# Optimization experiments

Measured on AMD Instinct MI355X. Metric: run time of the kernel, lower is better.

## Reference

```python
import jax, jax.numpy as jnp
import numpy as np

TEMP = 0.5
EPS = 1e-12  # matches torch F.normalize default eps


def _l2_normalize(x):
    n = jnp.sqrt(jnp.sum(x * x, axis=1, keepdims=True))
    return x / jnp.maximum(n, EPS)


def setup_inputs() -> dict:
    key = jax.random.key(0)
    k1, k2 = jax.random.split(key)
    B, D = 4096, 256
    return {
        "x_i": jax.random.normal(k1, (B, D), dtype=jnp.float32),
        "x_j": jax.random.normal(k2, (B, D), dtype=jnp.float32),
    }


def reference(x_i, x_j):
    B = x_i.shape[0]
    z = jnp.concatenate([_l2_normalize(x_i), _l2_normalize(x_j)], axis=0)  # [2B, D]
    # cosine similarity of normalized vectors == plain matmul
    sim = z @ z.T  # [2B, 2B]
    pos = jnp.concatenate([jnp.diagonal(sim, B), jnp.diagonal(sim, -B)], axis=0)  # [2B]
    neg_mask = 1.0 - jnp.eye(2 * B, dtype=sim.dtype)
    denom = jnp.sum(neg_mask * jnp.exp(sim / TEMP), axis=1)  # [2B]
    # -log(exp(pos/T) / denom) = -pos/T + log(denom)
    loss = jnp.sum(-(pos / TEMP) + jnp.log(denom)) / (2 * B)
    return loss
```

## Files before the change

### kernel.cpp

```cpp
#include <hip/hip_runtime.h>
#include <hip/hip_bf16.h>

#define B_ROWS 4096
#define NROWS  8192
#define D      256
#define NSEG   32
#define NBLK2  1024
#define TPP    130

typedef __attribute__((ext_vector_type(4))) float floatx4;

__global__ __launch_bounds__(256) void norm_pos_kernel(
    const float* __restrict__ xi, const float* __restrict__ xj,
    unsigned char* __restrict__ z, float* __restrict__ pos,
    float* __restrict__ rowsum, float* __restrict__ out,
    unsigned int* __restrict__ counter) {
    int gt = blockIdx.x * 256 + threadIdx.x;
    if (gt < NROWS) rowsum[gt] = 0.f;
    if (gt == 0) { out[0] = 0.f; counter[0] = 0u; }

    int p    = blockIdx.x * 4 + (threadIdx.x >> 6);
    int lane = threadIdx.x & 63;
    float4 v1 = ((const float4*)(xi + (size_t)p * D))[lane];
    float4 v2 = ((const float4*)(xj + (size_t)p * D))[lane];
    float ss1 = v1.x * v1.x + v1.y * v1.y + v1.z * v1.z + v1.w * v1.w;
    float ss2 = v2.x * v2.x + v2.y * v2.y + v2.z * v2.z + v2.w * v2.w;
#pragma unroll
    for (int off = 32; off > 0; off >>= 1) {
        ss1 += __shfl_xor(ss1, off);
        ss2 += __shfl_xor(ss2, off);
    }
    float sc1 = 1.0f / fmaxf(sqrtf(ss1), 1e-12f);
    float sc2 = 1.0f / fmaxf(sqrtf(ss2), 1e-12f);

    float n1x = v1.x * sc1, n1y = v1.y * sc1, n1z = v1.z * sc1, n1w = v1.w * sc1;
    float n2x = v2.x * sc2, n2y = v2.y * sc2, n2z = v2.z * sc2, n2w = v2.w * sc2;

    float dp = n1x * n2x + n1y * n2y + n1z * n2z + n1w * n2w;
#pragma unroll
    for (int off = 32; off > 0; off >>= 1) dp += __shfl_xor(dp, off);
    if (lane == 0) { pos[p] = dp; pos[p + B_ROWS] = dp; }

    int q1 = __builtin_amdgcn_cvt_pk_fp8_f32(n1x, n1y, 0, false);
    q1     = __builtin_amdgcn_cvt_pk_fp8_f32(n1z, n1w, q1, true);
    int q2 = __builtin_amdgcn_cvt_pk_fp8_f32(n2x, n2y, 0, false);
    q2     = __builtin_amdgcn_cvt_pk_fp8_f32(n2z, n2w, q2, true);
    ((int*)(z + (size_t)p * D))[lane]            = q1;
    ((int*)(z + (size_t)(p + B_ROWS) * D))[lane] = q2;
}

__global__ __launch_bounds__(256, 4) void sim_rowsum_kernel(
    const unsigned char* __restrict__ z, float* __restrict__ rowsum,
    const float* __restrict__ pos, unsigned int* __restrict__ counter,
    float* __restrict__ out) {
    __shared__ __align__(16) int4 Bbuf[2][1024];
    __shared__ unsigned int done_s;
    __shared__ float sdata[4];

    const int tid  = threadIdx.x;
    const int lane = tid & 63;
    const int w    = tid >> 6;
    const int lm   = lane & 15;
    const int lg   = lane >> 4;

    const int s  = blockIdx.x >> 5;
    const int q  = blockIdx.x & 31;
    const int L0 = 128 - 2 * s;
    const int cb = (q * TPP) >> 5;
    const int ce = ((q + 1) * TPP) >> 5;

    const int scol  = tid >> 2;
    const int spart = tid & 3;

    long long a[8][2];
    floatx4 acc[2][4];
    float rsacc[2][4];
    int4 pf[4];

#pragma unroll
    for (int mi = 0; mi < 2; mi++)
#pragma unroll
        for (int r = 0; r < 4; r++) rsacc[mi][r] = 0.f;

    auto decode = [&](int c, int& strip, int& colbase, int& cloc) {
        if (c < L0) { strip = s;      cloc = c; }
        else        { strip = 63 - s; cloc = c - L0; }
        colbase = strip * 128 + cloc * 64;
    };

    auto loadA = [&](int strip) {
#pragma unroll
        for (int kk = 0; kk < 8; kk++)
#pragma unroll
            for (int mi = 0; mi < 2; mi++)
                a[kk][mi] = *(const long long*)(
                    z + (size_t)(strip * 128 + w * 32 + mi * 16 + lm) * D +
                    kk * 32 + lg * 8);
    };

    auto flushRs = [&](int strip) {
#pragma unroll
        for (int mi = 0; mi < 2; mi++)
#pragma unroll
            for (int r = 0; r < 4; r++) {
                float v = rsacc[mi][r];
                v += __shfl_xor(v, 1); v += __shfl_xor(v, 2);
                v += __shfl_xor(v, 4); v += __shfl_xor(v, 8);
                if (lm == 0)
                    atomicAdd(&rowsum[strip * 128 + w * 32 + mi * 16 + lg * 4 + r], v);
                rsacc[mi][r] = 0.f;
            }
    };

    auto fetch = [&](int colbase) {
        const unsigned char* p = z + (size_t)(colbase + scol) * D + spart * 16;
#pragma unroll
        for (int j = 0; j < 4; j++) pf[j] = *(const int4*)(p + j * 64);
    };
    auto writeB = [&](int buf) {
#pragma unroll
        for (int j = 0; j < 4; j++)
            Bbuf[buf][(spart + 4 * j) * 64 + scol] = pf[j];
    };

    int strip, colbase, cloc;
    decode(cb, strip, colbase, cloc);
    int curstrip = strip;
    fetch(colbase);
    writeB(0);
    loadA(strip);
    __syncthreads();

    for (int c = cb; c < ce; c++) {
        const int buf = (c - cb) & 1;
        decode(c, strip, colbase, cloc);

        const bool hn = (c + 1 < ce);
        if (hn) {
            int ns, ncb, ncl;
            decode(c + 1, ns, ncb, ncl);
            fetch(ncb);
        }
        if (strip != curstrip) {
            flushRs(curstrip);
            loadA(strip);
            curstrip = strip;
        }

#pragma unroll
        for (int mi = 0; mi < 2; mi++)
#pragma unroll
            for (int ni = 0; ni < 4; ni++)
                acc[mi][ni] = (floatx4){0.f, 0.f, 0.f, 0.f};

        const char* bbase = (const char*)Bbuf[buf];
#pragma unroll
        for (int kk = 0; kk < 8; kk++) {
            long long b[4];
#pragma unroll
            for (int ni = 0; ni < 4; ni++)
                b[ni] = *(const long long*)(
                    bbase + (((kk * 2 + (lg >> 1)) * 64 + ni * 16 + lm) * 16) +
                    (lg & 1) * 8);
#pragma unroll
            for (int mi = 0; mi < 2; mi++)
#pragma unroll
                for (int ni = 0; ni < 4; ni++)
                    acc[mi][ni] = __builtin_amdgcn_mfma_f32_16x16x32_fp8_fp8(
                        a[kk][mi], b[ni], acc[mi][ni], 0, 0, 0);
        }

        const bool diagreg = (cloc < 2);
        float cs[4] = {0.f, 0.f, 0.f, 0.f};
        if (diagreg) {
            const int rowb = strip * 128 + w * 32 + lg * 4;
#pragma unroll
            for (int mi = 0; mi < 2; mi++)
#pragma unroll
                for (int ni = 0; ni < 4; ni++) {
                    const int gcol = colbase + ni * 16 + lm;
#pragma unroll
                    for (int r = 0; r < 4; r++) {
                        int grow = rowb + mi * 16 + r;
                        float e = (grow == gcol) ? 0.f
                                                 : __expf(2.0f * acc[mi][ni][r]);
                        rsacc[mi][r] += e;
                    }
                }
        } else {
#pragma unroll
            for (int mi = 0; mi < 2; mi++)
#pragma unroll
                for (int ni = 0; ni < 4; ni++)
#pragma unroll
                    for (int r = 0; r < 4; r++) {
                        float e = __expf(2.0f * acc[mi][ni][r]);
                        rsacc[mi][r] += e;
                        cs[ni]      += e;
                    }
#pragma unroll
            for (int ni = 0; ni < 4; ni++) {
                float v = cs[ni];
                v += __shfl_xor(v, 16); v += __shfl_xor(v, 32);
                if (lane < 16)
                    atomicAdd(&rowsum[colbase + ni * 16 + lane], v);
            }
        }

        if (hn) {
            writeB(buf ^ 1);
            __syncthreads();
        }
    }
    flushRs(curstrip);

    __syncthreads();
    if (tid == 0) {
        __threadfence();
        done_s = atomicAdd(counter, 1u);
    }
    __syncthreads();
    if (done_s == (unsigned int)(NBLK2 - 1)) {
        __threadfence();
        float acc_l = 0.f;
#pragma unroll 4
        for (int r = tid; r < NROWS; r += 256) {
            float rsv = __hip_atomic_load(&rowsum[r], __ATOMIC_RELAXED,
                                          __HIP_MEMORY_SCOPE_AGENT);
            acc_l += -2.0f * pos[r] + logf(rsv);
        }
#pragma unroll
        for (int off = 32; off > 0; off >>= 1) acc_l += __shfl_xor(acc_l, off);
        if (lane == 0) sdata[w] = acc_l;
        __syncthreads();
        if (tid == 0)
            out[0] = (sdata[0] + sdata[1] + sdata[2] + sdata[3]) / (float)NROWS;
    }
}

extern "C" void kernel_launch(void* const* d_in, const int* in_sizes, int n_in,
                              void* d_out, int out_size, void* d_ws, size_t ws_size,
                              hipStream_t stream) {
    const float* xi = (const float*)d_in[0];
    const float* xj = (const float*)d_in[1];
    float* out      = (float*)d_out;

    char* ws        = (char*)d_ws;
    unsigned char* z = (unsigned char*)ws;
    float* rowsum   = (float*)(ws + (size_t)NROWS * D);
    float* pos      = rowsum + NROWS;
    unsigned int* counter = (unsigned int*)(pos + NROWS);

    norm_pos_kernel<<<B_ROWS / 4, 256, 0, stream>>>(xi, xj, z, pos,
                                                    rowsum, out, counter);
    sim_rowsum_kernel<<<NBLK2, 256, 0, stream>>>(z, rowsum, pos, counter, out);
}
```

Baseline: 123.1 us.

## Restructure sim kernel to one 128x128 upper-triangle tile per block with swizzled LDS

```diff
diff --git a/kernel.cpp b/kernel.cpp
--- a/kernel.cpp
+++ b/kernel.cpp
@@ -4,9 +4,8 @@
 #define B_ROWS 4096
 #define NROWS  8192
 #define D      256
-#define NSEG   32
-#define NBLK2  1024
-#define TPP    130
+#define TILES  64
+#define NPAIRS 2080
 
 typedef __attribute__((ext_vector_type(4))) float floatx4;
 
@@ -49,11 +48,12 @@
     ((int*)(z + (size_t)(p + B_ROWS) * D))[lane] = q2;
 }
 
-__global__ __launch_bounds__(256, 4) void sim_rowsum_kernel(
+__global__ __launch_bounds__(256, 2) void sim_rowsum_kernel(
     const unsigned char* __restrict__ z, float* __restrict__ rowsum,
     const float* __restrict__ pos, unsigned int* __restrict__ counter,
     float* __restrict__ out) {
-    __shared__ __align__(16) int4 Bbuf[2][1024];
+    __shared__ __align__(16) char Ab[32768];
+    __shared__ __align__(16) char Bb[32768];
     __shared__ unsigned int done_s;
     __shared__ float sdata[4];
 
@@ -63,156 +63,132 @@
     const int lm   = lane & 15;
     const int lg   = lane >> 4;
 
-    const int s  = blockIdx.x >> 5;
-    const int q  = blockIdx.x & 31;
-    const int L0 = 128 - 2 * s;
-    const int cb = (q * TPP) >> 5;
-    const int ce = ((q + 1) * TPP) >> 5;
-
-    const int scol  = tid >> 2;
-    const int spart = tid & 3;
-
-    long long a[8][2];
-    floatx4 acc[2][4];
-    float rsacc[2][4];
-    int4 pf[4];
-
-#pragma unroll
-    for (int mi = 0; mi < 2; mi++)
-#pragma unroll
-        for (int r = 0; r < 4; r++) rsacc[mi][r] = 0.f;
-
-    auto decode = [&](int c, int& strip, int& colbase, int& cloc) {
-        if (c < L0) { strip = s;      cloc = c; }
-        else        { strip = 63 - s; cloc = c - L0; }
-        colbase = strip * 128 + cloc * 64;
-    };
-
-    auto loadA = [&](int strip) {
-#pragma unroll
-        for (int kk = 0; kk < 8; kk++)
-#pragma unroll
-            for (int mi = 0; mi < 2; mi++)
-                a[kk][mi] = *(const long long*)(
-                    z + (size_t)(strip * 128 + w * 32 + mi * 16 + lm) * D +
-                    kk * 32 + lg * 8);
-    };
-
-    auto flushRs = [&](int strip) {
-#pragma unroll
-        for (int mi = 0; mi < 2; mi++)
-#pragma unroll
-            for (int r = 0; r < 4; r++) {
-                float v = rsacc[mi][r];
-                v += __shfl_xor(v, 1); v += __shfl_xor(v, 2);
-                v += __shfl_xor(v, 4); v += __shfl_xor(v, 8);
-                if (lm == 0)
-                    atomicAdd(&rowsum[strip * 128 + w * 32 + mi * 16 + lg * 4 + r], v);
-                rsacc[mi][r] = 0.f;
+    int bid = blockIdx.x;
+    int ti  = (int)((129.0 - sqrt(16641.0 - 8.0 * (double)bid)) * 0.5);
+    while (ti > 0 && ti * TILES - ti * (ti - 1) / 2 > bid) ti--;
+    while ((ti + 1) * TILES - (ti + 1) * ti / 2 <= bid) ti++;
+    int tj = ti + (bid - (ti * TILES - ti * (ti - 1) / 2));
+    const int m0 = ti * 128, n0 = tj * 128;
+    const bool diag = (ti == tj);
+
+    const int wr = (w & 1) * 64;
+    const int wc = (w >> 1) * 64;
+
+    {
+        const int rb    = tid >> 2;
+        const int spart = tid & 3;
+        int4 pa[2][4], pb[2][4];
+#pragma unroll
+        for (int p = 0; p < 2; p++) {
+            const int row = rb + p * 64;
+            const unsigned char* pza = z + (size_t)(m0 + row) * D;
+            const unsigned char* pzb = z + (size_t)(n0 + row) * D;
+#pragma unroll
+            for (int j = 0; j < 4; j++) {
+                pa[p][j] = *(const int4*)(pza + spart * 16 + j * 64);
+                pb[p][j] = *(const int4*)(pzb + spart * 16 + j * 64);
             }
-    };
-
-    auto fetch = [&](int colbase) {
-        const unsigned char* p = z + (size_t)(colbase + scol) * D + spart * 16;
-#pragma unroll
-        for (int j = 0; j < 4; j++) pf[j] = *(const int4*)(p + j * 64);
-    };
-    auto writeB = [&](int buf) {
-#pragma unroll
-        for (int j = 0; j < 4; j++)
-            Bbuf[buf][(spart + 4 * j) * 64 + scol] = pf[j];
-    };
-
-    int strip, colbase, cloc;
-    decode(cb, strip, colbase, cloc);
-    int curstrip = strip;
-    fetch(colbase);
-    writeB(0);
-    loadA(strip);
+        }
+#pragma unroll
+        for (int p = 0; p < 2; p++) {
+            const int row = rb + p * 64;
+#pragma unroll
+            for (int j = 0; j < 4; j++) {
+                const int c16 = spart + 4 * j;
+                const int u   = c16 * 128 + (row ^ ((c16 & 1) * 16));
+                *(int4*)(Ab + u * 16) = pa[p][j];
+                *(int4*)(Bb + u * 16) = pb[p][j];
+            }
+        }
+    }
     __syncthreads();
 
-    for (int c = cb; c < ce; c++) {
-        const int buf = (c - cb) & 1;
-        decode(c, strip, colbase, cloc);
-
-        const bool hn = (c + 1 < ce);
-        if (hn) {
-            int ns, ncb, ncl;
-            decode(c + 1, ns, ncb, ncl);
-            fetch(ncb);
-        }
-        if (strip != curstrip) {
-            flushRs(curstrip);
-            loadA(strip);
-            curstrip = strip;
-        }
-
-#pragma unroll
-        for (int mi = 0; mi < 2; mi++)
+    floatx4 acc[4][4];
+#pragma unroll
+    for (int mi = 0; mi < 4; mi++)
+#pragma unroll
+        for (int ni = 0; ni < 4; ni++) acc[mi][ni] = (floatx4){0.f, 0.f, 0.f, 0.f};
+
+    const int h    = lg >> 1;
+    const int half = (lg & 1) * 8;
+
+#pragma unroll
+    for (int kk = 0; kk < 8; kk++) {
+        const int c16 = kk * 2 + h;
+        const int x   = (c16 & 1) * 16;
+        long long aF[4], bF[4];
+#pragma unroll
+        for (int mi = 0; mi < 4; mi++) {
+            const int u = c16 * 128 + ((wr + mi * 16 + lm) ^ x);
+            aF[mi] = *(const long long*)(Ab + u * 16 + half);
+        }
+#pragma unroll
+        for (int ni = 0; ni < 4; ni++) {
+            const int u = c16 * 128 + ((wc + ni * 16 + lm) ^ x);
+            bF[ni] = *(const long long*)(Bb + u * 16 + half);
+        }
+#pragma unroll
+        for (int mi = 0; mi < 4; mi++)
 #pragma unroll
             for (int ni = 0; ni < 4; ni++)
-                acc[mi][ni] = (floatx4){0.f, 0.f, 0.f, 0.f};
-
-        const char* bbase = (const char*)Bbuf[buf];
-#pragma unroll
-        for (int kk = 0; kk < 8; kk++) {
-            long long b[4];
+                acc[mi][ni] = __builtin_amdgcn_mfma_f32_16x16x32_fp8_fp8(
+                    aF[mi], bF[ni], acc[mi][ni], 0, 0, 0);
+    }
+
+    float rs[4][4], cs[4];
+#pragma unroll
+    for (int mi = 0; mi < 4; mi++)
+#pragma unroll
+        for (int r = 0; r < 4; r++) rs[mi][r] = 0.f;
+#pragma unroll
+    for (int ni = 0; ni < 4; ni++) cs[ni] = 0.f;
+
+    if (diag) {
+        const int rowb = m0 + wr + lg * 4;
+#pragma unroll
+        for (int mi = 0; mi < 4; mi++)
+#pragma unroll
+            for (int ni = 0; ni < 4; ni++) {
+                const int gcol = n0 + wc + ni * 16 + lm;
+#pragma unroll
+                for (int r = 0; r < 4; r++) {
+                    const int grow = rowb + mi * 16 + r;
+                    float e = (grow == gcol) ? 0.f : __expf(2.0f * acc[mi][ni][r]);
+                    rs[mi][r] += e;
+                }
+            }
+    } else {
+#pragma unroll
+        for (int mi = 0; mi < 4; mi++)
 #pragma unroll
             for (int ni = 0; ni < 4; ni++)
-                b[ni] = *(const long long*)(
-                    bbase + (((kk * 2 + (lg >> 1)) * 64 + ni * 16 + lm) * 16) +
-                    (lg & 1) * 8);
-#pragma unroll
-            for (int mi = 0; mi < 2; mi++)
-#pragma unroll
-                for (int ni = 0; ni < 4; ni++)
-                    acc[mi][ni] = __builtin_amdgcn_mfma_f32_16x16x32_fp8_fp8(
-                        a[kk][mi], b[ni], acc[mi][ni], 0, 0, 0);
-        }
-
-        const bool diagreg = (cloc < 2);
-        float cs[4] = {0.f, 0.f, 0.f, 0.f};
-        if (diagreg) {
-            const int rowb = strip * 128 + w * 32 + lg * 4;
-#pragma unroll
-            for (int mi = 0; mi < 2; mi++)
-#pragma unroll
-                for (int ni = 0; ni < 4; ni++) {
-                    const int gcol = colbase + ni * 16 + lm;
-#pragma unroll
-                    for (int r = 0; r < 4; r++) {
-                        int grow = rowb + mi * 16 + r;
-                        float e = (grow == gcol) ? 0.f
-                                                 : __expf(2.0f * acc[mi][ni][r]);
-                        rsacc[mi][r] += e;
-                    }
+#pragma unroll
+                for (int r = 0; r < 4; r++) {
+                    float e = __expf(2.0f * acc[mi][ni][r]);
+                    rs[mi][r] += e;
+                    cs[ni]    += e;
                 }
-        } else {
-#pragma unroll
-            for (int mi = 0; mi < 2; mi++)
-#pragma unroll
-                for (int ni = 0; ni < 4; ni++)
-#pragma unroll
-                    for (int r = 0; r < 4; r++) {
-                        float e = __expf(2.0f * acc[mi][ni][r]);
-                        rsacc[mi][r] += e;
-                        cs[ni]      += e;
-                    }
-#pragma unroll
-            for (int ni = 0; ni < 4; ni++) {
-                float v = cs[ni];
-                v += __shfl_xor(v, 16); v += __shfl_xor(v, 32);
-                if (lane < 16)
-                    atomicAdd(&rowsum[colbase + ni * 16 + lane], v);
-            }
-        }
-
-        if (hn) {
-            writeB(buf ^ 1);
-            __syncthreads();
-        }
-    }
-    flushRs(curstrip);
+    }
+
+#pragma unroll
+    for (int mi = 0; mi < 4; mi++)
+#pragma unroll
+        for (int r = 0; r < 4; r++) {
+            float v = rs[mi][r];
+            v += __shfl_xor(v, 1); v += __shfl_xor(v, 2);
+            v += __shfl_xor(v, 4); v += __shfl_xor(v, 8);
+            if (lm == 0)
+                atomicAdd(&rowsum[m0 + wr + mi * 16 + lg * 4 + r], v);
+        }
+    if (!diag) {
+#pragma unroll
+        for (int ni = 0; ni < 4; ni++) {
+            float v = cs[ni];
+            v += __shfl_xor(v, 16); v += __shfl_xor(v, 32);
+            if (lane < 16)
+                atomicAdd(&rowsum[n0 + wc + ni * 16 + lane], v);
+        }
+    }
 
     __syncthreads();
     if (tid == 0) {
@@ -220,7 +196,7 @@
         done_s = atomicAdd(counter, 1u);
     }
     __syncthreads();
-    if (done_s == (unsigned int)(NBLK2 - 1)) {
+    if (done_s == (unsigned int)(NPAIRS - 1)) {
         __threadfence();
         float acc_l = 0.f;
 #pragma unroll 4
@@ -245,13 +221,13 @@
     const float* xj = (const float*)d_in[1];
     float* out      = (float*)d_out;
 
-    char* ws        = (char*)d_ws;
+    char* ws         = (char*)d_ws;
     unsigned char* z = (unsigned char*)ws;
-    float* rowsum   = (float*)(ws + (size_t)NROWS * D);
-    float* pos      = rowsum + NROWS;
+    float* rowsum    = (float*)(ws + (size_t)NROWS * D);
+    float* pos       = rowsum + NROWS;
     unsigned int* counter = (unsigned int*)(pos + NROWS);
 
     norm_pos_kernel<<<B_ROWS / 4, 256, 0, stream>>>(xi, xj, z, pos,
                                                     rowsum, out, counter);
-    sim_rowsum_kernel<<<NBLK2, 256, 0, stream>>>(z, rowsum, pos, counter, out);
+    sim_rowsum_kernel<<<NPAIRS, 256, 0, stream>>>(z, rowsum, pos, counter, out);
 }
```

New measurement: 137.8 us. 12.0% more time.
